# Optimization experiments

Hardware: AMD Instinct MI355X
Metric: run time of the kernel (lower is better)

## Reference

```python
import jax, jax.numpy as jnp
import numpy as np

N = 8192
D = 1024
TAU = 1.0
ALPHA = 1.0
BETA = 0.0


def setup_inputs() -> dict:
    key = jax.random.key(0)
    z = jax.random.normal(key, (2 * N, D), dtype=jnp.float32)
    return {"z": z}


def reference(z):
    n = z.shape[0] // 2
    x1, x2 = z[:n], z[n:]
    x1_abs = jnp.linalg.norm(x1, axis=1)  # [N]
    x2_abs = jnp.linalg.norm(x2, axis=1)  # [N]
    # cosine similarity matrix / tau: [N, N]
    matrix = jnp.einsum('ik,jk->ij', x1, x2) / (x1_abs[:, None] * x2_abs[None, :]) / TAU
    pos_sim = jnp.diagonal(matrix)                     # [N]
    neg_sim = (matrix.sum(axis=1) - pos_sim) / (n - 1)  # [N]
    sim_matrix = jnp.exp(matrix)
    pos = jnp.diagonal(sim_matrix)
    p_ij = pos / (sim_matrix.sum(axis=1) - pos)
    alpha = jax.lax.stop_gradient(p_ij - 1.0 + ALPHA)
    loss = -jnp.log(p_ij) - alpha * pos_sim + neg_sim * BETA
    return (loss.mean(), p_ij.mean())
```

## Files before the change

### kernel.cpp

```cpp
#include <hip/hip_runtime.h>
#include <hip/hip_bf16.h>

typedef __hip_bfloat16 bf16_t;
typedef __attribute__((ext_vector_type(8))) short  s16x8;
typedef __attribute__((ext_vector_type(4))) float  f32x4;

#define N_ROWS 8192
#define D_DIM  1024

#define GLOAD_LDS16(g, l)                                                     \
  __builtin_amdgcn_global_load_lds(                                           \
      (const __attribute__((address_space(1))) void*)(g),                     \
      (__attribute__((address_space(3))) void*)(l), 16, 0, 0)

#define WAITCNT_VM(n) asm volatile("s_waitcnt vmcnt(" #n ")" ::: "memory")
#define BARRIER_()                                                            \
  do {                                                                        \
    asm volatile("" ::: "memory");                                            \
    __builtin_amdgcn_s_barrier();                                             \
    asm volatile("" ::: "memory");                                            \
  } while (0)

struct alignas(8) bf16x4_s { bf16_t x, y, z, w; };

__global__ void __launch_bounds__(256) normalize_kernel(
    const float* __restrict__ z, bf16_t* __restrict__ out,
    float* __restrict__ rowsum) {
  const int t = threadIdx.x;
  if (blockIdx.x < 32) rowsum[blockIdx.x * 256 + t] = 0.f;
  const int row  = blockIdx.x * 4 + (t >> 6);
  const int lane = t & 63;
  const float4* rp = (const float4*)(z + (size_t)row * D_DIM);
  float4 v[4];
#pragma unroll
  for (int j = 0; j < 4; ++j) v[j] = rp[lane + 64 * j];
  float ss = 0.f;
#pragma unroll
  for (int j = 0; j < 4; ++j)
    ss += v[j].x * v[j].x + v[j].y * v[j].y + v[j].z * v[j].z + v[j].w * v[j].w;
  ss += __shfl_xor(ss, 1);
  ss += __shfl_xor(ss, 2);
  ss += __shfl_xor(ss, 4);
  ss += __shfl_xor(ss, 8);
  ss += __shfl_xor(ss, 16);
  ss += __shfl_xor(ss, 32);
  const float rn = rsqrtf(ss);
  bf16x4_s* op = (bf16x4_s*)(out + (size_t)row * D_DIM);
#pragma unroll
  for (int j = 0; j < 4; ++j) {
    bf16x4_s o;
    o.x = __float2bfloat16(v[j].x * rn);
    o.y = __float2bfloat16(v[j].y * rn);
    o.z = __float2bfloat16(v[j].z * rn);
    o.w = __float2bfloat16(v[j].w * rn);
    op[lane + 64 * j] = o;
  }
}

__global__ void __launch_bounds__(512, 2) simexp_gemm(
    const bf16_t* __restrict__ A, const bf16_t* __restrict__ B,
    float* __restrict__ rowsum, float* __restrict__ pos_sim) {
  constexpr int SLOT = 32768;
  __shared__ bf16_t lds[2 * SLOT];

  const int t    = threadIdx.x;
  const int w    = t >> 6;
  const int lane = t & 63;
  const int wr   = w >> 2;
  const int wc   = w & 3;
  const int rb   = blockIdx.y, cb = blockIdx.x;
  const int row0 = rb * 256, col0 = cb * 256;

  const int srow = t >> 2;
  const int scol = ((t & 3) ^ ((t >> 3) & 3)) * 8;
  const int ldst = w * 512;

#define STGA(s, kh, Tt)                                                       \
  do {                                                                        \
    const int gc = (Tt) * 64 + (kh) * 32 + scol;                              \
    GLOAD_LDS16(A + (size_t)(row0 + srow) * D_DIM + gc,                       \
                lds + (s) * SLOT + (kh) * 8192 + ldst);                       \
    GLOAD_LDS16(A + (size_t)(row0 + 128 + srow) * D_DIM + gc,                 \
                lds + (s) * SLOT + (kh) * 8192 + 4096 + ldst);                \
  } while (0)
#define STGB(s, kh, Tt)                                                       \
  do {                                                                        \
    const int gc = (Tt) * 64 + (kh) * 32 + scol;                              \
    GLOAD_LDS16(B + (size_t)(col0 + srow) * D_DIM + gc,                       \
                lds + (s) * SLOT + 16384 + (kh) * 8192 + ldst);               \
    GLOAD_LDS16(B + (size_t)(col0 + 128 + srow) * D_DIM + gc,                 \
                lds + (s) * SLOT + 16384 + (kh) * 8192 + 4096 + ldst);        \
  } while (0)

  int offA[8], offB[4];
#pragma unroll
  for (int m = 0; m < 8; ++m) {
    const int r = wr * 128 + m * 16 + (lane & 15);
    offA[m] = r * 32 + (((lane >> 4) ^ ((r >> 1) & 3)) * 8);
  }
#pragma unroll
  for (int n = 0; n < 4; ++n) {
    const int r = wc * 64 + n * 16 + (lane & 15);
    offB[n] = r * 32 + (((lane >> 4) ^ ((r >> 1) & 3)) * 8);
  }

  f32x4 acc[8][4];
#pragma unroll
  for (int m = 0; m < 8; ++m)
#pragma unroll
    for (int n = 0; n < 4; ++n) acc[m][n] = (f32x4){0.f, 0.f, 0.f, 0.f};

#define LOADB4_(s, kh)                                                        \
  do {                                                                        \
    _Pragma("unroll") for (int n = 0; n < 4; ++n) bfv[n] =                    \
        *(const s16x8*)&lds[(s) * SLOT + 16384 + (kh) * 8192 + offB[n]];      \
  } while (0)
#define LOADA4_(s, kh, mb)                                                    \
  do {                                                                        \
    _Pragma("unroll") for (int m = 0; m < 4; ++m) afv[m] =                    \
        *(const s16x8*)&lds[(s) * SLOT + (kh) * 8192 + offA[(mb) + m]];       \
  } while (0)
#define MFMA16_(mb)                                                           \
  do {                                                                        \
    __builtin_amdgcn_s_setprio(1);                                            \
    _Pragma("unroll") for (int m = 0; m < 4; ++m)                             \
        _Pragma("unroll") for (int n = 0; n < 4; ++n) acc[(mb) + m][n] =      \
            __builtin_amdgcn_mfma_f32_16x16x32_bf16(afv[m], bfv[n],           \
                                                    acc[(mb) + m][n], 0, 0, 0); \
    __builtin_amdgcn_s_setprio(0);                                            \
  } while (0)

#define KWIN(s, S1, S2, S3, S4, W2, W4)                                       \
  do {                                                                        \
    s16x8 bfv[4], afv[4];                                                     \
    LOADB4_(s, 0); LOADA4_(s, 0, 0); S1; MFMA16_(0); BARRIER_();              \
    LOADA4_(s, 0, 4); S2; MFMA16_(4); W2; BARRIER_();                         \
    LOADB4_(s, 1); LOADA4_(s, 1, 0); S3; MFMA16_(0); BARRIER_();              \
    LOADA4_(s, 1, 4); S4; MFMA16_(4); W4; BARRIER_();                         \
  } while (0)

  STGA(0, 0, 0); STGB(0, 0, 0);
  STGA(0, 1, 0); STGB(0, 1, 0);
  STGA(1, 0, 1); STGB(1, 0, 1);
  WAITCNT_VM(8);
  BARRIER_();

#pragma unroll 1
  for (int i = 0; i < 7; ++i) {
    const int T = 2 * i;
    KWIN(0, STGA(1, 1, T + 1), STGB(1, 1, T + 1),
            STGA(0, 0, T + 2), STGB(0, 0, T + 2),
            WAITCNT_VM(8), WAITCNT_VM(8));
    KWIN(1, STGA(0, 1, T + 2), STGB(0, 1, T + 2),
            STGA(1, 0, T + 3), STGB(1, 0, T + 3),
            WAITCNT_VM(8), WAITCNT_VM(8));
  }
  KWIN(0, STGA(1, 1, 15), STGB(1, 1, 15), , , WAITCNT_VM(8), WAITCNT_VM(4));
  KWIN(1, , , , , WAITCNT_VM(0), );

  if (rb == cb) {
#pragma unroll
    for (int m = 0; m < 8; ++m)
#pragma unroll
      for (int n = 0; n < 4; ++n)
#pragma unroll
        for (int r = 0; r < 4; ++r) {
          const int grow = wr * 128 + m * 16 + (lane >> 4) * 4 + r;
          const int gcol = wc * 64 + n * 16 + (lane & 15);
          if (grow == gcol) pos_sim[row0 + grow] = acc[m][n][r];
        }
  }

  __syncthreads();
  float* red = (float*)lds;
#pragma unroll
  for (int m = 0; m < 8; ++m)
#pragma unroll
    for (int r = 0; r < 4; ++r) {
      float s = 0.f;
#pragma unroll
      for (int n = 0; n < 4; ++n) s += __expf(acc[m][n][r]);
      s += __shfl_xor(s, 1);
      s += __shfl_xor(s, 2);
      s += __shfl_xor(s, 4);
      s += __shfl_xor(s, 8);
      if ((lane & 15) == 0) {
        const int row_local = wr * 128 + m * 16 + (lane >> 4) * 4 + r;
        red[wc * 256 + row_local] = s;
      }
    }
  __syncthreads();
  if (t < 256) {
    const float s4 = red[t] + red[256 + t] + red[512 + t] + red[768 + t];
    atomicAdd(&rowsum[row0 + t], s4);
  }
#undef STGA
#undef STGB
#undef LOADB4_
#undef LOADA4_
#undef MFMA16_
#undef KWIN
}

__global__ void __launch_bounds__(256) finalize_kernel(
    const float* __restrict__ rowsum, const float* __restrict__ pos_sim,
    float* __restrict__ out) {
  const int t = threadIdx.x;
  double lsum = 0.0, psum = 0.0;
  for (int i = t; i < N_ROWS; i += 256) {
    const float ps    = pos_sim[i];
    const float pos   = expf(ps);
    const float denom = rowsum[i] - pos;
    const float p     = pos / denom;
    lsum += (double)(-logf(p) - p * ps);
    psum += (double)p;
  }
  for (int off = 32; off; off >>= 1) {
    lsum += __shfl_down(lsum, off);
    psum += __shfl_down(psum, off);
  }
  __shared__ double sl[4], sp[4];
  const int wv = t >> 6, ln = t & 63;
  if (ln == 0) { sl[wv] = lsum; sp[wv] = psum; }
  __syncthreads();
  if (t == 0) {
    const double L = sl[0] + sl[1] + sl[2] + sl[3];
    const double P = sp[0] + sp[1] + sp[2] + sp[3];
    out[0] = (float)(L / N_ROWS);
    out[1] = (float)(P / N_ROWS);
  }
}

extern "C" void kernel_launch(void* const* d_in, const int* in_sizes, int n_in,
                              void* d_out, int out_size, void* d_ws,
                              size_t ws_size, hipStream_t stream) {
  const float* z = (const float*)d_in[0];
  float* out = (float*)d_out;

  char* ws = (char*)d_ws;
  bf16_t* AB = (bf16_t*)ws;
  float* rowsum  = (float*)(ws + (size_t)2 * N_ROWS * D_DIM * sizeof(bf16_t));
  float* pos_sim = rowsum + N_ROWS;

  normalize_kernel<<<2 * N_ROWS / 4, 256, 0, stream>>>(z, AB, rowsum);

  bf16_t* Amat = AB;
  bf16_t* Bmat = AB + (size_t)N_ROWS * D_DIM;
  dim3 grid(N_ROWS / 256, N_ROWS / 256);
  simexp_gemm<<<grid, 512, 0, stream>>>(Amat, Bmat, rowsum, pos_sim);

  finalize_kernel<<<1, 256, 0, stream>>>(rowsum, pos_sim, out);
}
```

Measured before the change: 230.0 us.

## Quantize normalized rows to FP8 e4m3 and use FP8 MFMA in similarity GEMM

The normalize kernel now writes unit-norm rows as FP8 e4m3 bytes instead of bf16. The GEMM uses the fp8 16x16x32 MFMA on 8-byte operands, with K tiles of 128 bytes staged in four quarters and a new LDS swizzle. This halves operand bytes and uses the higher-throughput FP8 matrix path, so global traffic and MFMA time should drop. The cost is lower precision in the cosine similarities, which are then exponentiated and summed, so the loss values may drift from the reference.

```diff
diff --git a/kernel.cpp b/kernel.cpp
--- a/kernel.cpp
+++ b/kernel.cpp
@@ -1,9 +1,9 @@
 #include <hip/hip_runtime.h>
 #include <hip/hip_bf16.h>
-
-typedef __hip_bfloat16 bf16_t;
-typedef __attribute__((ext_vector_type(8))) short  s16x8;
-typedef __attribute__((ext_vector_type(4))) float  f32x4;
+#include <hip/hip_fp8.h>
+
+typedef __attribute__((ext_vector_type(4))) float f32x4;
+typedef unsigned char u8;
 
 #define N_ROWS 8192
 #define D_DIM  1024
@@ -21,19 +21,17 @@
     asm volatile("" ::: "memory");                                            \
   } while (0)
 
-struct alignas(8) bf16x4_s { bf16_t x, y, z, w; };
-
-__global__ void __launch_bounds__(256) normalize_kernel(
-    const float* __restrict__ z, bf16_t* __restrict__ out,
+__global__ void __launch_bounds__(256) normq_kernel(
+    const float* __restrict__ z, u8* __restrict__ out,
     float* __restrict__ rowsum) {
   const int t = threadIdx.x;
   if (blockIdx.x < 32) rowsum[blockIdx.x * 256 + t] = 0.f;
   const int row  = blockIdx.x * 4 + (t >> 6);
   const int lane = t & 63;
-  const float4* rp = (const float4*)(z + (size_t)row * D_DIM);
+  const float4* rp = (const float4*)(z + (size_t)row * D_DIM) + lane * 4;
   float4 v[4];
 #pragma unroll
-  for (int j = 0; j < 4; ++j) v[j] = rp[lane + 64 * j];
+  for (int j = 0; j < 4; ++j) v[j] = rp[j];
   float ss = 0.f;
 #pragma unroll
   for (int j = 0; j < 4; ++j)
@@ -45,23 +43,22 @@
   ss += __shfl_xor(ss, 16);
   ss += __shfl_xor(ss, 32);
   const float rn = rsqrtf(ss);
-  bf16x4_s* op = (bf16x4_s*)(out + (size_t)row * D_DIM);
+  uint wds[4];
 #pragma unroll
   for (int j = 0; j < 4; ++j) {
-    bf16x4_s o;
-    o.x = __float2bfloat16(v[j].x * rn);
-    o.y = __float2bfloat16(v[j].y * rn);
-    o.z = __float2bfloat16(v[j].z * rn);
-    o.w = __float2bfloat16(v[j].w * rn);
-    op[lane + 64 * j] = o;
-  }
+    __hip_fp8_e4m3 q0(v[j].x * rn), q1(v[j].y * rn);
+    __hip_fp8_e4m3 q2(v[j].z * rn), q3(v[j].w * rn);
+    wds[j] = (uint)q0.__x | ((uint)q1.__x << 8) | ((uint)q2.__x << 16) |
+             ((uint)q3.__x << 24);
+  }
+  uint4 o; o.x = wds[0]; o.y = wds[1]; o.z = wds[2]; o.w = wds[3];
+  *(uint4*)(out + (size_t)row * D_DIM + lane * 16) = o;
 }
 
 __global__ void __launch_bounds__(512, 2) simexp_gemm(
-    const bf16_t* __restrict__ A, const bf16_t* __restrict__ B,
+    const u8* __restrict__ A, const u8* __restrict__ B,
     float* __restrict__ rowsum, float* __restrict__ pos_sim) {
-  constexpr int SLOT = 32768;
-  __shared__ bf16_t lds[2 * SLOT];
+  __shared__ u8 lds[131072];
 
   const int t    = threadIdx.x;
   const int w    = t >> 6;
@@ -71,37 +68,28 @@
   const int rb   = blockIdx.y, cb = blockIdx.x;
   const int row0 = rb * 256, col0 = cb * 256;
 
-  const int srow = t >> 2;
-  const int scol = ((t & 3) ^ ((t >> 3) & 3)) * 8;
-  const int ldst = w * 512;
-
-#define STGA(s, kh, Tt)                                                       \
-  do {                                                                        \
-    const int gc = (Tt) * 64 + (kh) * 32 + scol;                              \
-    GLOAD_LDS16(A + (size_t)(row0 + srow) * D_DIM + gc,                       \
-                lds + (s) * SLOT + (kh) * 8192 + ldst);                       \
-    GLOAD_LDS16(A + (size_t)(row0 + 128 + srow) * D_DIM + gc,                 \
-                lds + (s) * SLOT + (kh) * 8192 + 4096 + ldst);                \
-  } while (0)
-#define STGB(s, kh, Tt)                                                       \
-  do {                                                                        \
-    const int gc = (Tt) * 64 + (kh) * 32 + scol;                              \
-    GLOAD_LDS16(B + (size_t)(col0 + srow) * D_DIM + gc,                       \
-                lds + (s) * SLOT + 16384 + (kh) * 8192 + ldst);               \
-    GLOAD_LDS16(B + (size_t)(col0 + 128 + srow) * D_DIM + gc,                 \
-                lds + (s) * SLOT + 16384 + (kh) * 8192 + 4096 + ldst);        \
-  } while (0)
-
+  const int srow  = t >> 1;
+  const int scolq = ((t & 1) ^ ((srow >> 2) & 1)) * 16;
+  const int ldst  = w * 1024;
+
+#define STGA(ss, q, T)                                                        \
+  GLOAD_LDS16(A + (size_t)(row0 + srow) * D_DIM + (T) * 128 + (q) * 32 + scolq,\
+              lds + (ss) * 65536 + (q) * 8192 + ldst)
+#define STGB(ss, q, T)                                                        \
+  GLOAD_LDS16(B + (size_t)(col0 + srow) * D_DIM + (T) * 128 + (q) * 32 + scolq,\
+              lds + (ss) * 65536 + 32768 + (q) * 8192 + ldst)
+
+  const int c8 = lane >> 4;
   int offA[8], offB[4];
 #pragma unroll
   for (int m = 0; m < 8; ++m) {
     const int r = wr * 128 + m * 16 + (lane & 15);
-    offA[m] = r * 32 + (((lane >> 4) ^ ((r >> 1) & 3)) * 8);
+    offA[m] = r * 32 + ((c8 ^ (((r >> 2) & 1) << 1)) * 8);
   }
 #pragma unroll
   for (int n = 0; n < 4; ++n) {
     const int r = wc * 64 + n * 16 + (lane & 15);
-    offB[n] = r * 32 + (((lane >> 4) ^ ((r >> 1) & 3)) * 8);
+    offB[n] = r * 32 + ((c8 ^ (((r >> 2) & 1) << 1)) * 8);
   }
 
   f32x4 acc[8][4];
@@ -110,53 +98,48 @@
 #pragma unroll
     for (int n = 0; n < 4; ++n) acc[m][n] = (f32x4){0.f, 0.f, 0.f, 0.f};
 
-#define LOADB4_(s, kh)                                                        \
+#define KQ2(ss, q, WN, SA, SB)                                                \
   do {                                                                        \
+    WAITCNT_VM(WN);                                                           \
+    BARRIER_();                                                               \
+    long bfv[4], afv[4];                                                      \
     _Pragma("unroll") for (int n = 0; n < 4; ++n) bfv[n] =                    \
-        *(const s16x8*)&lds[(s) * SLOT + 16384 + (kh) * 8192 + offB[n]];      \
-  } while (0)
-#define LOADA4_(s, kh, mb)                                                    \
-  do {                                                                        \
+        *(const long*)(lds + (ss) * 65536 + 32768 + (q) * 8192 + offB[n]);    \
     _Pragma("unroll") for (int m = 0; m < 4; ++m) afv[m] =                    \
-        *(const s16x8*)&lds[(s) * SLOT + (kh) * 8192 + offA[(mb) + m]];       \
-  } while (0)
-#define MFMA16_(mb)                                                           \
-  do {                                                                        \
+        *(const long*)(lds + (ss) * 65536 + (q) * 8192 + offA[m]);            \
+    SA;                                                                       \
     __builtin_amdgcn_s_setprio(1);                                            \
     _Pragma("unroll") for (int m = 0; m < 4; ++m)                             \
-        _Pragma("unroll") for (int n = 0; n < 4; ++n) acc[(mb) + m][n] =      \
-            __builtin_amdgcn_mfma_f32_16x16x32_bf16(afv[m], bfv[n],           \
-                                                    acc[(mb) + m][n], 0, 0, 0); \
+        _Pragma("unroll") for (int n = 0; n < 4; ++n) acc[m][n] =             \
+            __builtin_amdgcn_mfma_f32_16x16x32_fp8_fp8(afv[m], bfv[n],        \
+                                                       acc[m][n], 0, 0, 0);   \
+    __builtin_amdgcn_s_setprio(0);                                            \
+    _Pragma("unroll") for (int m = 0; m < 4; ++m) afv[m] =                    \
+        *(const long*)(lds + (ss) * 65536 + (q) * 8192 + offA[4 + m]);        \
+    SB;                                                                       \
+    __builtin_amdgcn_s_setprio(1);                                            \
+    _Pragma("unroll") for (int m = 0; m < 4; ++m)                             \
+        _Pragma("unroll") for (int n = 0; n < 4; ++n) acc[4 + m][n] =         \
+            __builtin_amdgcn_mfma_f32_16x16x32_fp8_fp8(afv[m], bfv[n],        \
+                                                       acc[4 + m][n], 0, 0, 0);\
     __builtin_amdgcn_s_setprio(0);                                            \
   } while (0)
 
-#define KWIN(s, S1, S2, S3, S4, W2, W4)                                       \
-  do {                                                                        \
-    s16x8 bfv[4], afv[4];                                                     \
-    LOADB4_(s, 0); LOADA4_(s, 0, 0); S1; MFMA16_(0); BARRIER_();              \
-    LOADA4_(s, 0, 4); S2; MFMA16_(4); W2; BARRIER_();                         \
-    LOADB4_(s, 1); LOADA4_(s, 1, 0); S3; MFMA16_(0); BARRIER_();              \
-    LOADA4_(s, 1, 4); S4; MFMA16_(4); W4; BARRIER_();                         \
-  } while (0)
-
-  STGA(0, 0, 0); STGB(0, 0, 0);
-  STGA(0, 1, 0); STGB(0, 1, 0);
-  STGA(1, 0, 1); STGB(1, 0, 1);
-  WAITCNT_VM(8);
-  BARRIER_();
+#pragma unroll
+  for (int q = 0; q < 4; ++q) { STGA(0, q, 0); STGB(0, q, 0); }
 
 #pragma unroll 1
-  for (int i = 0; i < 7; ++i) {
-    const int T = 2 * i;
-    KWIN(0, STGA(1, 1, T + 1), STGB(1, 1, T + 1),
-            STGA(0, 0, T + 2), STGB(0, 0, T + 2),
-            WAITCNT_VM(8), WAITCNT_VM(8));
-    KWIN(1, STGA(0, 1, T + 2), STGB(0, 1, T + 2),
-            STGA(1, 0, T + 3), STGB(1, 0, T + 3),
-            WAITCNT_VM(8), WAITCNT_VM(8));
-  }
-  KWIN(0, STGA(1, 1, 15), STGB(1, 1, 15), , , WAITCNT_VM(8), WAITCNT_VM(4));
-  KWIN(1, , , , , WAITCNT_VM(0), );
+  for (int T = 0; T < 7; ++T) {
+    const int ss = T & 1, ns = ss ^ 1;
+    KQ2(ss, 0, 6, STGA(ns, 0, T + 1), STGB(ns, 0, T + 1));
+    KQ2(ss, 1, 6, STGA(ns, 1, T + 1), STGB(ns, 1, T + 1));
+    KQ2(ss, 2, 6, STGA(ns, 2, T + 1), STGB(ns, 2, T + 1));
+    KQ2(ss, 3, 6, STGA(ns, 3, T + 1), STGB(ns, 3, T + 1));
+  }
+  KQ2(1, 0, 6, , );
+  KQ2(1, 1, 4, , );
+  KQ2(1, 2, 2, , );
+  KQ2(1, 3, 0, , );
 
   if (rb == cb) {
 #pragma unroll
@@ -196,10 +179,7 @@
   }
 #undef STGA
 #undef STGB
-#undef LOADB4_
-#undef LOADA4_
-#undef MFMA16_
-#undef KWIN
+#undef KQ2
 }
 
 __global__ void __launch_bounds__(256) finalize_kernel(
@@ -238,14 +218,14 @@
   float* out = (float*)d_out;
 
   char* ws = (char*)d_ws;
-  bf16_t* AB = (bf16_t*)ws;
-  float* rowsum  = (float*)(ws + (size_t)2 * N_ROWS * D_DIM * sizeof(bf16_t));
+  u8* AB = (u8*)ws;
+  float* rowsum  = (float*)(ws + (size_t)2 * N_ROWS * D_DIM);
   float* pos_sim = rowsum + N_ROWS;
 
-  normalize_kernel<<<2 * N_ROWS / 4, 256, 0, stream>>>(z, AB, rowsum);
-
-  bf16_t* Amat = AB;
-  bf16_t* Bmat = AB + (size_t)N_ROWS * D_DIM;
+  normq_kernel<<<2 * N_ROWS / 4, 256, 0, stream>>>(z, AB, rowsum);
+
+  u8* Amat = AB;
+  u8* Bmat = AB + (size_t)N_ROWS * D_DIM;
   dim3 grid(N_ROWS / 256, N_ROWS / 256);
   simexp_gemm<<<grid, 512, 0, stream>>>(Amat, Bmat, rowsum, pos_sim);
 
```

After: 220.1 us. 4.3% less time.
